# Kernel optimization log

Hardware: AMD Instinct MI355X
Metric: run time of the kernel (lower is better)

## Reference

```python
import jax, jax.numpy as jnp
import numpy as np

N_EMBD = 1024
N_HEAD = 16
HEAD_DIM = N_EMBD // N_HEAD
EPS = 1e-5


def _gelu_tanh(x):
    c = jnp.sqrt(jnp.asarray(2.0 / jnp.pi, x.dtype))
    return 0.5 * x * (1.0 + jnp.tanh(c * (x + 0.044715 * x ** 3)))


def _layernorm(x, scale, shift):
    # torch.var defaults to unbiased (ddof=1) -- replicate exactly
    mean = jnp.mean(x, axis=-1, keepdims=True)
    var = jnp.var(x, axis=-1, keepdims=True, ddof=1)
    return (x - mean) / jnp.sqrt(var + EPS) * scale + shift


def setup_inputs() -> dict:
    key = jax.random.key(0)
    ks = jax.random.split(key, 8)
    d, h = N_EMBD, 4 * N_EMBD
    s = 0.02
    return {
        "x": jax.random.normal(ks[0], (2, 2048, d), jnp.float32),
        "ln1_scale": jnp.ones((d,), jnp.float32),
        "ln1_shift": jnp.zeros((d,), jnp.float32),
        "wq": jax.random.normal(ks[1], (d, d), jnp.float32) * s,
        "wk": jax.random.normal(ks[2], (d, d), jnp.float32) * s,
        "wv": jax.random.normal(ks[3], (d, d), jnp.float32) * s,
        "w_out": jax.random.normal(ks[4], (d, d), jnp.float32) * s,
        "b_out": jnp.zeros((d,), jnp.float32),
        "ln2_scale": jnp.ones((d,), jnp.float32),
        "ln2_shift": jnp.zeros((d,), jnp.float32),
        "w1": jax.random.normal(ks[5], (d, h), jnp.float32) * s,
        "b1": jnp.zeros((h,), jnp.float32),
        "w2": jax.random.normal(ks[6], (h, d), jnp.float32) * s,
        "b2": jnp.zeros((d,), jnp.float32),
    }


def reference(x, ln1_scale, ln1_shift, wq, wk, wv, w_out, b_out,
              ln2_scale, ln2_shift, w1, b1, w2, b2):
    B, S, D = x.shape
    out = _layernorm(x, ln1_scale, ln1_shift)

    # qkv projections (no bias), split heads: [B, H, S, hd]
    q = (out @ wq).reshape(B, S, N_HEAD, HEAD_DIM).transpose(0, 2, 1, 3)
    k = (out @ wk).reshape(B, S, N_HEAD, HEAD_DIM).transpose(0, 2, 1, 3)
    v = (out @ wv).reshape(B, S, N_HEAD, HEAD_DIM).transpose(0, 2, 1, 3)

    scores = jnp.einsum("bhqd,bhkd->bhqk", q, k)
    causal = jnp.triu(jnp.ones((S, S), bool), k=1)
    # original masks BEFORE scaling; -inf / sqrt(d) is still -inf
    scores = jnp.where(causal, -jnp.inf, scores)
    weights = jax.nn.softmax(scores / jnp.sqrt(jnp.asarray(HEAD_DIM, scores.dtype)), axis=-1)
    ctx = jnp.einsum("bhqk,bhkd->bqhd", weights, v).reshape(B, S, D)
    attn_out = ctx @ w_out + b_out

    out = attn_out + x  # dropout is identity (rate 0)
    shortcut = out
    out = _layernorm(out, ln2_scale, ln2_shift)
    out = _gelu_tanh(out @ w1 + b1) @ w2 + b2
    return out + shortcut
```

## Files before the change

### kernel.cpp

```cpp
#include <hip/hip_runtime.h>
#include <stdint.h>
#include <math.h>

using bf16x8 = __attribute__((ext_vector_type(8))) short;
using f32x4  = __attribute__((ext_vector_type(4))) float;

#define MFMA16 __builtin_amdgcn_mfma_f32_16x16x32_bf16

__device__ __forceinline__ uint16_t f2b(float f) {
    union { float f; uint32_t i; } v; v.f = f;
    uint32_t r = v.i + 0x7fffu + ((v.i >> 16) & 1u);
    return (uint16_t)(r >> 16);
}
__device__ __forceinline__ float b2f(uint16_t u) {
    union { uint32_t i; float f; } v; v.i = ((uint32_t)u) << 16; return v.f;
}

typedef const __attribute__((address_space(1))) void gvoid;
typedef __attribute__((address_space(3))) void svoid;

__global__ __launch_bounds__(256) void fill_zero(float* __restrict__ o, int n) {
    int i = (blockIdx.x * 256 + threadIdx.x) * 4;
    if (i < n) *(float4*)(o + i) = make_float4(0.f, 0.f, 0.f, 0.f);
}

__global__ __launch_bounds__(256) void transpose_qkvo(
    const float* __restrict__ wq, const float* __restrict__ wk,
    const float* __restrict__ wv, const float* __restrict__ wo,
    uint16_t* __restrict__ wqkvT, uint16_t* __restrict__ woT)
{
    const int D = 1024;
    int z = blockIdx.z;
    const float* W = (z == 0) ? wq : (z == 1) ? wk : (z == 2) ? wv : wo;
    uint16_t* Wt = (z < 3) ? (wqkvT + (size_t)z * D * D) : woT;
    __shared__ uint16_t t[32][33];
    int n0 = blockIdx.x * 32, k0 = blockIdx.y * 32;
    int tx = threadIdx.x, ty = threadIdx.y;
    #pragma unroll
    for (int i = ty; i < 32; i += 8)
        t[i][tx] = f2b(W[(size_t)(k0 + i) * D + (n0 + tx)]);
    __syncthreads();
    #pragma unroll
    for (int i = ty; i < 32; i += 8)
        Wt[(size_t)(n0 + i) * D + (k0 + tx)] = t[tx][i];
}

__global__ __launch_bounds__(256) void transpose_f2b(
    const float* __restrict__ W, uint16_t* __restrict__ Wt, int K, int N)
{
    __shared__ uint16_t t[32][33];
    int n0 = blockIdx.x * 32, k0 = blockIdx.y * 32;
    int tx = threadIdx.x, ty = threadIdx.y;
    #pragma unroll
    for (int i = ty; i < 32; i += 8)
        t[i][tx] = f2b(W[(size_t)(k0 + i) * N + (n0 + tx)]);
    __syncthreads();
    #pragma unroll
    for (int i = ty; i < 32; i += 8)
        Wt[(size_t)(n0 + i) * K + (k0 + tx)] = t[tx][i];
}

__global__ __launch_bounds__(256) void ln_kernel(
    const float* __restrict__ src, const float* __restrict__ scale,
    const float* __restrict__ shift, uint16_t* __restrict__ out)
{
    const int D = 1024;
    int row = blockIdx.x, t = threadIdx.x;
    float4 f = *((const float4*)(src + (size_t)row * D) + t);
    float v[4] = {f.x, f.y, f.z, f.w};
    float s1 = v[0] + v[1] + v[2] + v[3];
    float s2 = v[0]*v[0] + v[1]*v[1] + v[2]*v[2] + v[3]*v[3];
    #pragma unroll
    for (int off = 32; off; off >>= 1) {
        s1 += __shfl_xor(s1, off);
        s2 += __shfl_xor(s2, off);
    }
    __shared__ float red[2][4];
    __shared__ float stat[2];
    int wid = t >> 6, lane = t & 63;
    if (lane == 0) { red[0][wid] = s1; red[1][wid] = s2; }
    __syncthreads();
    if (t == 0) {
        float S1 = red[0][0] + red[0][1] + red[0][2] + red[0][3];
        float S2 = red[1][0] + red[1][1] + red[1][2] + red[1][3];
        float mean = S1 / (float)D;
        float var  = fmaxf((S2 - mean * S1) / (float)(D - 1), 0.f);
        stat[0] = mean; stat[1] = rsqrtf(var + 1e-5f);
    }
    __syncthreads();
    float mean = stat[0], rstd = stat[1];
    float4 sc = *((const float4*)scale + t);
    float4 sh = *((const float4*)shift + t);
    uint16_t o[4];
    o[0] = f2b((v[0] - mean) * rstd * sc.x + sh.x);
    o[1] = f2b((v[1] - mean) * rstd * sc.y + sh.y);
    o[2] = f2b((v[2] - mean) * rstd * sc.z + sh.z);
    o[3] = f2b((v[3] - mean) * rstd * sc.w + sh.w);
    uint2 st;
    st.x = (uint32_t)o[0] | ((uint32_t)o[1] << 16);
    st.y = (uint32_t)o[2] | ((uint32_t)o[3] << 16);
    *(uint2*)(out + (size_t)row * D + t * 4) = st;
}

__global__ __launch_bounds__(256) void combine2(
    float* __restrict__ dst, const float* __restrict__ part0,
    const float* __restrict__ resid, const float* __restrict__ bias)
{
    const int D = 1024;
    size_t o = (size_t)blockIdx.x * D + threadIdx.x * 4;
    float4 a = *(float4*)(dst + o);
    float4 b = *(const float4*)(part0 + o);
    float4 c = *(const float4*)(resid + o);
    float4 bv = *((const float4*)bias + threadIdx.x);
    a.x += b.x + c.x + bv.x;
    a.y += b.y + c.y + bv.y;
    a.z += b.z + c.z + bv.z;
    a.w += b.w + c.w + bv.w;
    *(float4*)(dst + o) = a;
}

__global__ __launch_bounds__(256) void combine2ln(
    float* __restrict__ res1, const float* __restrict__ part0,
    const float* __restrict__ x, const float* __restrict__ bo,
    const float* __restrict__ scale, const float* __restrict__ shift,
    uint16_t* __restrict__ out)
{
    const int D = 1024;
    int row = blockIdx.x, t = threadIdx.x;
    size_t o = (size_t)row * D + t * 4;
    float4 a = *(float4*)(res1 + o);
    float4 b = *(const float4*)(part0 + o);
    float4 c = *(const float4*)(x + o);
    float4 bv = *((const float4*)bo + t);
    float v[4] = {a.x + b.x + c.x + bv.x, a.y + b.y + c.y + bv.y,
                  a.z + b.z + c.z + bv.z, a.w + b.w + c.w + bv.w};
    *(float4*)(res1 + o) = make_float4(v[0], v[1], v[2], v[3]);

    float s1 = v[0] + v[1] + v[2] + v[3];
    float s2 = v[0]*v[0] + v[1]*v[1] + v[2]*v[2] + v[3]*v[3];
    #pragma unroll
    for (int off = 32; off; off >>= 1) {
        s1 += __shfl_xor(s1, off);
        s2 += __shfl_xor(s2, off);
    }
    __shared__ float red[2][4];
    __shared__ float stat[2];
    int wid = t >> 6, lane = t & 63;
    if (lane == 0) { red[0][wid] = s1; red[1][wid] = s2; }
    __syncthreads();
    if (t == 0) {
        float S1 = red[0][0] + red[0][1] + red[0][2] + red[0][3];
        float S2 = red[1][0] + red[1][1] + red[1][2] + red[1][3];
        float mean = S1 / (float)D;
        float var  = fmaxf((S2 - mean * S1) / (float)(D - 1), 0.f);
        stat[0] = mean; stat[1] = rsqrtf(var + 1e-5f);
    }
    __syncthreads();
    float mean = stat[0], rstd = stat[1];
    float4 sc = *((const float4*)scale + t);
    float4 sh = *((const float4*)shift + t);
    uint16_t ob[4];
    ob[0] = f2b((v[0] - mean) * rstd * sc.x + sh.x);
    ob[1] = f2b((v[1] - mean) * rstd * sc.y + sh.y);
    ob[2] = f2b((v[2] - mean) * rstd * sc.z + sh.z);
    ob[3] = f2b((v[3] - mean) * rstd * sc.w + sh.w);
    uint2 st;
    st.x = (uint32_t)ob[0] | ((uint32_t)ob[1] << 16);
    st.y = (uint32_t)ob[2] | ((uint32_t)ob[3] << 16);
    *(uint2*)(out + (size_t)row * D + t * 4) = st;
}

__device__ __forceinline__ void stage128(
    const uint16_t* __restrict__ A, const uint16_t* __restrict__ Bt,
    uint16_t* As, uint16_t* Bs,
    int m0, int n0, int lda, int kk, int w, int l)
{
    int srow = l >> 3;
    int sc = ((l & 7) ^ srow) << 3;
    #pragma unroll
    for (int p = 0; p < 4; ++p) {
        int rbase = w * 32 + p * 8;
        const uint16_t* ga = A  + (size_t)(m0 + rbase + srow) * lda + kk + sc;
        const uint16_t* gb = Bt + (size_t)(n0 + rbase + srow) * lda + kk + sc;
        __builtin_amdgcn_global_load_lds((gvoid*)ga, (svoid*)(As + rbase * 64), 16, 0, 0);
        __builtin_amdgcn_global_load_lds((gvoid*)gb, (svoid*)(Bs + rbase * 64), 16, 0, 0);
    }
}

__device__ __forceinline__ void comp128(
    const uint16_t* As, const uint16_t* Bs, f32x4 (&acc)[4][4],
    int mo, int no, int quad, int ln, int sw)
{
    #pragma unroll
    for (int s = 0; s < 2; ++s) {
        int cc = ((s * 64 + quad * 16) ^ sw) >> 1;
        bf16x8 af[4], bf[4];
        #pragma unroll
        for (int i = 0; i < 4; ++i)
            af[i] = *(const bf16x8*)(As + (mo + i * 16 + ln) * 64 + cc);
        #pragma unroll
        for (int i = 0; i < 4; ++i)
            bf[i] = *(const bf16x8*)(Bs + (no + i * 16 + ln) * 64 + cc);
        #pragma unroll
        for (int mi = 0; mi < 4; ++mi)
            #pragma unroll
            for (int ni = 0; ni < 4; ++ni)
                acc[mi][ni] = MFMA16(af[mi], bf[ni], acc[mi][ni], 0, 0, 0);
    }
}

template <int EPI>
__global__ __launch_bounds__(256) void gemm128(
    const uint16_t* __restrict__ A, const uint16_t* __restrict__ Bt,
    const float* __restrict__ bias, const float* __restrict__ resid,
    void* __restrict__ outp, void* __restrict__ out2,
    int M, int N, int K, int lda)
{
    __shared__ __align__(16) uint16_t As0[128 * 64];
    __shared__ __align__(16) uint16_t As1[128 * 64];
    __shared__ __align__(16) uint16_t Bs0[128 * 64];
    __shared__ __align__(16) uint16_t Bs1[128 * 64];
    int tid = threadIdx.x;
    int w = tid >> 6, l = tid & 63;
    int quad = l >> 4, ln = l & 15;
    int sw = (ln & 7) << 4;

    int Nt = gridDim.x, Mt = gridDim.y;
    int L0 = blockIdx.y * Nt + blockIdx.x;
    int nb = Nt * Mt;
    int L = (L0 & 7) * (nb >> 3) + (L0 >> 3);
    const int GROUP = 8;
    int nig = GROUP * Nt;
    int gid = L / nig;
    int fm = gid * GROUP;
    int gsz = min(Mt - fm, GROUP);
    int rem = L - gid * nig;
    int pid_m = fm + rem % gsz;
    int pid_n = rem / gsz;
    int n0 = pid_n * 128, m0 = pid_m * 128;
    int kofs = (EPI == 5) ? blockIdx.z * K : 0;

    int mo = (w & 1) * 64, no = (w >> 1) * 64;

    f32x4 acc[4][4];
    #pragma unroll
    for (int mi = 0; mi < 4; ++mi)
        #pragma unroll
        for (int ni = 0; ni < 4; ++ni) acc[mi][ni] = (f32x4){0.f, 0.f, 0.f, 0.f};

    int nk = K >> 6;
    stage128(A, Bt, As0, Bs0, m0, n0, lda, kofs, w, l);
    __syncthreads();

    for (int t = 0; t + 2 <= nk; t += 2) {
        stage128(A, Bt, As1, Bs1, m0, n0, lda, kofs + (t + 1) * 64, w, l);
        comp128(As0, Bs0, acc, mo, no, quad, ln, sw);
        __syncthreads();
        if (t + 2 < nk)
            stage128(A, Bt, As0, Bs0, m0, n0, lda, kofs + (t + 2) * 64, w, l);
        comp128(As1, Bs1, acc, mo, no, quad, ln, sw);
        if (t + 2 < nk) __syncthreads();
    }

    float* pout = (EPI == 5) ? (blockIdx.z ? (float*)out2 : (float*)outp) : (float*)outp;

    #pragma unroll
    for (int ni = 0; ni < 4; ++ni) {
        int col = n0 + no + ni * 16 + ln;
        if (EPI == 4 && col >= 2048) {
            int hh = (col - 2048) >> 6, d = (col - 2048) & 63;
            #pragma unroll
            for (int mi = 0; mi < 4; ++mi) {
                int tok = m0 + mo + mi * 16 + quad * 4;
                int bat = tok >> 11, s = tok & 2047;
                uint16_t pk[4];
                #pragma unroll
                for (int r = 0; r < 4; ++r) pk[r] = f2b(acc[mi][ni][r]);
                uint2 st;
                st.x = (uint32_t)pk[0] | ((uint32_t)pk[1] << 16);
                st.y = (uint32_t)pk[2] | ((uint32_t)pk[3] << 16);
                *(uint2*)((uint16_t*)out2 +
                          ((size_t)(bat * 16 + hh) * 64 + d) * 2048 + s) = st;
            }
            continue;
        }
        float bv = (EPI == 1 || EPI == 2) ? bias[col] : 0.f;
        #pragma unroll
        for (int mi = 0; mi < 4; ++mi) {
            #pragma unroll
            for (int r = 0; r < 4; ++r) {
                int row = m0 + mo + mi * 16 + quad * 4 + r;
                float vacc = acc[mi][ni][r] + bv;
                if (EPI == 1) {
                    size_t idx = (size_t)row * N + col;
                    ((float*)outp)[idx] = vacc + resid[idx];
                } else if (EPI == 5) {
                    pout[(size_t)row * N + col] = vacc;
                } else if (EPI == 2) {
                    float x = vacc;
                    float u = 0.7978845608028654f * (x + 0.044715f * x * x * x);
                    float g = x / (1.f + __expf(-2.f * u));
                    ((uint16_t*)outp)[(size_t)row * N + col] = f2b(g);
                } else {
                    float vs = (col < 1024) ? vacc * 0.125f : vacc;
                    ((uint16_t*)outp)[(size_t)(col >> 10) * M * 1024 +
                                      (size_t)row * 1024 + (col & 1023)] = f2b(vs);
                }
            }
        }
    }
}

__device__ __forceinline__ void stage_half(
    const uint16_t* __restrict__ Mat, uint16_t* lds,
    int panel0, int lda, int kk, int w, int l)
{
    #pragma unroll
    for (int i = 0; i < 2; ++i) {
        int idx = i * 512 + w * 64 + l;
        int row = idx >> 3;
        int sc = ((idx & 7) ^ (row & 7)) << 3;
        const uint16_t* g = Mat + (size_t)(panel0 + row) * lda + kk + sc;
        __builtin_amdgcn_global_load_lds(
            (gvoid*)g, (svoid*)(lds + (i * 512 + w * 64) * 8), 16, 0, 0);
    }
}

template <int EPI>
__global__ __launch_bounds__(512, 2) void gemm256(
    const uint16_t* __restrict__ A, const uint16_t* __restrict__ Bt,
    const float* __restrict__ bias, const float* __restrict__ resid,
    void* __restrict__ outp, void* __restrict__ out2,
    int M, int N, int K, int lda)
{
    __shared__ __align__(16) uint16_t AsL[32768];
    __shared__ __align__(16) uint16_t BsL[32768];
    int tid = threadIdx.x;
    int w = tid >> 6, l = tid & 63;
    int quad = l >> 4, ln = l & 15;
    int wr = w >> 2, wc = w & 3;
    int sw = (ln & 7) << 4;
    int cc0 = ((quad * 16) ^ sw) >> 1;
    int cc1 = ((64 + quad * 16) ^ sw) >> 1;

    int Nt = gridDim.x, Mt = gridDim.y;
    int L0 = blockIdx.y * Nt + blockIdx.x;
    int nb = Nt * Mt;
    int L = (L0 & 7) * (nb >> 3) + (L0 >> 3);
    const int GROUP = 8;
    int nig = GROUP * Nt;
    int gid = L / nig;
    int fm = gid * GROUP;
    int gsz = min(Mt - fm, GROUP);
    int rem = L - gid * nig;
    int pid_m = fm + rem % gsz;
    int pid_n = rem / gsz;
    int n0 = pid_n * 256, m0 = pid_m * 256;
    int kofs = (EPI == 5) ? blockIdx.z * K : 0;

    f32x4 acc[8][4];
    #pragma unroll
    for (int mi = 0; mi < 8; ++mi)
        #pragma unroll
        for (int ni = 0; ni < 4; ++ni) acc[mi][ni] = (f32x4){0.f, 0.f, 0.f, 0.f};

    int nk = K >> 6;

    stage_half(Bt, BsL,         n0,       lda, kofs,      w, l);
    stage_half(A,  AsL,         m0,       lda, kofs,      w, l);
    stage_half(A,  AsL + 8192,  m0 + 128, lda, kofs,      w, l);
    stage_half(Bt, BsL + 8192,  n0 + 128, lda, kofs,      w, l);
    stage_half(Bt, BsL + 16384, n0,       lda, kofs + 64, w, l);
    stage_half(A,  AsL + 16384, m0,       lda, kofs + 64, w, l);
    asm volatile("s_waitcnt vmcnt(4)" ::: "memory");
    __builtin_amdgcn_s_barrier();
    __builtin_amdgcn_sched_barrier(0);

    for (int t = 0; t < nk; ++t) {
        int b = t & 1;
        const uint16_t* Ar = AsL + b * 16384 + wr * 8192;
        const uint16_t* Br = BsL + b * 16384 + (wc >> 1) * 8192 + (wc & 1) * 4096;
        uint16_t* stA1 = AsL + (b ^ 1) * 16384 + 8192;
        uint16_t* stB1 = BsL + (b ^ 1) * 16384 + 8192;
        uint16_t* stA0 = AsL + b * 16384;
        uint16_t* stB0 = BsL + b * 16384;
        int kk1 = kofs + (t + 1) * 64;
        int kk2 = kofs + (t + 2) * 64;
        bool g1 = (t + 1) < nk, g2 = (t + 2) < nk;

        bf16x8 af[4][2], bL[2][2], bH[2][2];

        #pragma unroll
        for (int mi = 0; mi < 4; ++mi) {
            af[mi][0] = *(const bf16x8*)(Ar + (mi * 16 + ln) * 64 + cc0);
            af[mi][1] = *(const bf16x8*)(Ar + (mi * 16 + ln) * 64 + cc1);
        }
        #pragma unroll
        for (int ni = 0; ni < 2; ++ni) {
            bL[ni][0] = *(const bf16x8*)(Br + (ni * 16 + ln) * 64 + cc0);
            bL[ni][1] = *(const bf16x8*)(Br + (ni * 16 + ln) * 64 + cc1);
        }
        if (g1) stage_half(A, stA1, m0 + 128, lda, kk1, w, l);
        __builtin_amdgcn_s_barrier();
        __builtin_amdgcn_sched_barrier(0);
        __builtin_amdgcn_s_setprio(1);
        #pragma unroll
        for (int mi = 0; mi < 4; ++mi)
            #pragma unroll
            for (int ni = 0; ni < 2; ++ni) {
                acc[mi][ni] = MFMA16(af[mi][0], bL[ni][0], acc[mi][ni], 0, 0, 0);
                acc[mi][ni] = MFMA16(af[mi][1], bL[ni][1], acc[mi][ni], 0, 0, 0);
            }
        __builtin_amdgcn_s_setprio(0);
        __builtin_amdgcn_s_barrier();
        __builtin_amdgcn_sched_barrier(0);

        #pragma unroll
        for (int ni = 0; ni < 2; ++ni) {
            bH[ni][0] = *(const bf16x8*)(Br + ((ni + 2) * 16 + ln) * 64 + cc0);
            bH[ni][1] = *(const bf16x8*)(Br + ((ni + 2) * 16 + ln) * 64 + cc1);
        }
        if (g1) stage_half(Bt, stB1, n0 + 128, lda, kk1, w, l);
        __builtin_amdgcn_s_barrier();
        __builtin_amdgcn_sched_barrier(0);
        __builtin_amdgcn_s_setprio(1);
        #pragma unroll
        for (int mi = 0; mi < 4; ++mi)
            #pragma unroll
            for (int ni = 0; ni < 2; ++ni) {
                acc[mi][ni + 2] = MFMA16(af[mi][0], bH[ni][0], acc[mi][ni + 2], 0, 0, 0);
                acc[mi][ni + 2] = MFMA16(af[mi][1], bH[ni][1], acc[mi][ni + 2], 0, 0, 0);
            }
        __builtin_amdgcn_s_setprio(0);
        __builtin_amdgcn_s_barrier();
        __builtin_amdgcn_sched_barrier(0);

        #pragma unroll
        for (int mi = 0; mi < 4; ++mi) {
            af[mi][0] = *(const bf16x8*)(Ar + ((mi + 4) * 16 + ln) * 64 + cc0);
            af[mi][1] = *(const bf16x8*)(Ar + ((mi + 4) * 16 + ln) * 64 + cc1);
        }
        if (g2) stage_half(Bt, stB0, n0, lda, kk2, w, l);
        __builtin_amdgcn_s_barrier();
        __builtin_amdgcn_sched_barrier(0);
        __builtin_amdgcn_s_setprio(1);
        #pragma unroll
        for (int mi = 0; mi < 4; ++mi)
            #pragma unroll
            for (int ni = 0; ni < 2; ++ni) {
                acc[mi + 4][ni] = MFMA16(af[mi][0], bL[ni][0], acc[mi + 4][ni], 0, 0, 0);
                acc[mi + 4][ni] = MFMA16(af[mi][1], bL[ni][1], acc[mi + 4][ni], 0, 0, 0);
            }
        __builtin_amdgcn_s_setprio(0);
        __builtin_amdgcn_s_barrier();
        __builtin_amdgcn_sched_barrier(0);

        if (g2) {
            stage_half(A, stA0, m0, lda, kk2, w, l);
            asm volatile("s_waitcnt vmcnt(4)" ::: "memory");
        } else if (g1) {
            asm volatile("s_waitcnt vmcnt(0)" ::: "memory");
        }
        __builtin_amdgcn_s_barrier();
        __builtin_amdgcn_sched_barrier(0);
        __builtin_amdgcn_s_setprio(1);
        #pragma unroll
        for (int mi = 0; mi < 4; ++mi)
            #pragma unroll
            for (int ni = 0; ni < 2; ++ni) {
                acc[mi + 4][ni + 2] = MFMA16(af[mi][0], bH[ni][0], acc[mi + 4][ni + 2], 0, 0, 0);
                acc[mi + 4][ni + 2] = MFMA16(af[mi][1], bH[ni][1], acc[mi + 4][ni + 2], 0, 0, 0);
            }
        __builtin_amdgcn_s_setprio(0);
        __builtin_amdgcn_s_barrier();
        __builtin_amdgcn_sched_barrier(0);
    }

    float* pout = (EPI == 5) ? (blockIdx.z ? (float*)out2 : (float*)outp) : (float*)outp;

    #pragma unroll
    for (int ni = 0; ni < 4; ++ni) {
        int col = n0 + wc * 64 + ni * 16 + ln;
        if (EPI == 4 && col >= 2048) {
            int hh = (col - 2048) >> 6, d = (col - 2048) & 63;
            #pragma unroll
            for (int mi = 0; mi < 8; ++mi) {
                int tok = m0 + wr * 128 + mi * 16 + quad * 4;
                int bat = tok >> 11, s = tok & 2047;
                uint16_t pk[4];
                #pragma unroll
                for (int r = 0; r < 4; ++r) pk[r] = f2b(acc[mi][ni][r]);
                uint2 st;
                st.x = (uint32_t)pk[0] | ((uint32_t)pk[1] << 16);
                st.y = (uint32_t)pk[2] | ((uint32_t)pk[3] << 16);
                *(uint2*)((uint16_t*)out2 +
                          ((size_t)(bat * 16 + hh) * 64 + d) * 2048 + s) = st;
            }
            continue;
        }
        float bv = (EPI == 2) ? bias[col] : 0.f;
        #pragma unroll
        for (int mi = 0; mi < 8; ++mi) {
            #pragma unroll
            for (int r = 0; r < 4; ++r) {
                int row = m0 + wr * 128 + mi * 16 + quad * 4 + r;
                float vacc = acc[mi][ni][r] + bv;
                if (EPI == 5) {
                    pout[(size_t)row * N + col] = vacc;
                } else if (EPI == 2) {
                    float x = vacc;
                    float u = 0.7978845608028654f * (x + 0.044715f * x * x * x);
                    float g = x / (1.f + __expf(-2.f * u));
                    ((uint16_t*)outp)[(size_t)row * N + col] = f2b(g);
                } else {
                    float vs = (col < 1024) ? vacc * 0.125f : vacc;
                    ((uint16_t*)outp)[(size_t)(col >> 10) * M * 1024 +
                                      (size_t)row * 1024 + (col & 1023)] = f2b(vs);
                }
            }
        }
    }
}

__device__ __forceinline__ void attn_tile(
    const uint16_t* __restrict__ Kl, const uint16_t* __restrict__ Vl,
    uint16_t* __restrict__ Pw,
    bf16x8 qf0, bf16x8 qf1,
    float* l_r, f32x4* o_acc,
    int qw, int kv0, bool diag, int quad, int ln)
{
    const int LW = 72;
    f32x4 sf[4];
    #pragma unroll
    for (int nt2 = 0; nt2 < 4; ++nt2) {
        const uint16_t* kp = Kl + (nt2 * 16 + ln) * LW + quad * 8;
        bf16x8 k0 = *(const bf16x8*)(kp);
        bf16x8 k1 = *(const bf16x8*)(kp + 32);
        f32x4 z = {0.f, 0.f, 0.f, 0.f};
        z = MFMA16(qf0, k0, z, 0, 0, 0);
        z = MFMA16(qf1, k1, z, 0, 0, 0);
        sf[nt2] = z;
    }
    #pragma unroll
    for (int r = 0; r < 4; ++r) {
        float ps = 0.f;
        if (diag) {
            int qrow = qw + quad * 4 + r;
            #pragma unroll
            for (int nt2 = 0; nt2 < 4; ++nt2) {
                int kv = kv0 + nt2 * 16 + ln;
                float pv = (kv <= qrow) ? __expf(sf[nt2][r]) : 0.f;
                sf[nt2][r] = pv;
                ps += pv;
            }
        } else {
            #pragma unroll
            for (int nt2 = 0; nt2 < 4; ++nt2) {
                float pv = __expf(sf[nt2][r]);
                sf[nt2][r] = pv;
                ps += pv;
            }
        }
        ps += __shfl_xor(ps, 1);
        ps += __shfl_xor(ps, 2);
        ps += __shfl_xor(ps, 4);
        ps += __shfl_xor(ps, 8);
        l_r[r] += ps;
    }
    #pragma unroll
    for (int nt2 = 0; nt2 < 4; ++nt2) {
        int gl = nt2 * 2 + (ln >> 3);
        int off = ln & 7;
        #pragma unroll
        for (int r = 0; r < 4; ++r) {
            int row = quad * 4 + r;
            int p = gl ^ ((quad << 1) ^ r);
            Pw[row * 64 + p * 8 + off] = f2b(sf[nt2][r]);
        }
    }
    int swl = ((ln >> 2) << 1) ^ (ln & 3);
    int g0 = quad ^ swl;
    int g1 = (quad + 4) ^ swl;
    bf16x8 p0 = *(const bf16x8*)(Pw + ln * 64 + g0 * 8);
    bf16x8 p1 = *(const bf16x8*)(Pw + ln * 64 + g1 * 8);
    #pragma unroll
    for (int dt = 0; dt < 4; ++dt) {
        const uint16_t* vp = Vl + (dt * 16 + ln) * LW + quad * 8;
        bf16x8 v0 = *(const bf16x8*)(vp);
        bf16x8 v1 = *(const bf16x8*)(vp + 32);
        o_acc[dt] = MFMA16(p0, v0, o_acc[dt], 0, 0, 0);
        o_acc[dt] = MFMA16(p1, v1, o_acc[dt], 0, 0, 0);
    }
}

__global__ __launch_bounds__(256) void attn_flash(
    const uint16_t* __restrict__ Q,
    const uint16_t* __restrict__ K,
    const uint16_t* __restrict__ Vt,
    uint16_t* __restrict__ O,
    int B, int S, int H)
{
    const int D = 1024;
    const int LW = 72;
    __shared__ uint16_t Kl[64 * 72];
    __shared__ uint16_t Vl[64 * 72];
    __shared__ uint16_t Pl[64 * 64];

    int tid = threadIdx.x;
    int w = tid >> 6, l = tid & 63;
    int quad = l >> 4, ln = l & 15;

    int NT = S / 64;
    int h = blockIdx.y, b = blockIdx.z;
    int qt = ((h >> 3) & 1) ? blockIdx.x : (NT - 1 - blockIdx.x);
    size_t rb = (size_t)b * S;

    int qw = qt * 64 + w * 16;

    const uint16_t* qp = Q + (rb + qw + ln) * D + h * 64 + quad * 8;
    bf16x8 q0 = *(const bf16x8*)(qp);
    bf16x8 q1 = *(const bf16x8*)(qp + 32);

    const uint16_t* Kbase = K + rb * D + h * 64;
    const uint16_t* Vbase = Vt + (size_t)(b * H + h) * 64 * S;
    uint16_t* Pw = Pl + w * 16 * 64;

    int sr0 = tid >> 3,         sc0 = (tid & 7) * 8;
    int sr1 = (256 + tid) >> 3, sc1 = ((256 + tid) & 7) * 8;

    float lr[4] = {0.f, 0.f, 0.f, 0.f};
    f32x4 oa[4];
    #pragma unroll
    for (int dt = 0; dt < 4; ++dt)
        oa[dt] = (f32x4){0.f, 0.f, 0.f, 0.f};

    uint4 kr0 = *(const uint4*)(Kbase + (size_t)sr0 * D + sc0);
    uint4 kr1 = *(const uint4*)(Kbase + (size_t)sr1 * D + sc1);
    uint4 vr0 = *(const uint4*)(Vbase + (size_t)sr0 * S + sc0);
    uint4 vr1 = *(const uint4*)(Vbase + (size_t)sr1 * S + sc1);

    for (int t = 0; t <= qt; ++t) {
        __syncthreads();
        *(uint4*)(Kl + sr0 * LW + sc0) = kr0;
        *(uint4*)(Kl + sr1 * LW + sc1) = kr1;
        *(uint4*)(Vl + sr0 * LW + sc0) = vr0;
        *(uint4*)(Vl + sr1 * LW + sc1) = vr1;
        __syncthreads();
        if (t < qt) {
            int kv1 = (t + 1) * 64;
            kr0 = *(const uint4*)(Kbase + (size_t)(kv1 + sr0) * D + sc0);
            kr1 = *(const uint4*)(Kbase + (size_t)(kv1 + sr1) * D + sc1);
            vr0 = *(const uint4*)(Vbase + (size_t)sr0 * S + kv1 + sc0);
            vr1 = *(const uint4*)(Vbase + (size_t)sr1 * S + kv1 + sc1);
        }
        attn_tile(Kl, Vl, Pw, q0, q1, lr, oa, qw, t * 64, t == qt, quad, ln);
    }

    #pragma unroll
    for (int r = 0; r < 4; ++r) {
        float inv = 1.f / lr[r];
        uint16_t* op = O + (rb + qw + quad * 4 + r) * D + h * 64 + ln;
        #pragma unroll
        for (int dt = 0; dt < 4; ++dt)
            op[dt * 16] = f2b(oa[dt][r] * inv);
    }
}

extern "C" void kernel_launch(void* const* d_in, const int* in_sizes, int n_in,
                              void* d_out, int out_size, void* d_ws, size_t ws_size,
                              hipStream_t stream)
{
    (void)in_sizes; (void)n_in;
    const int B = 2, S = 2048, D = 1024, H = 16, F = 4096;
    const int M = B * S;
    const size_t MB = 1u << 20;

    const float* x    = (const float*)d_in[0];
    const float* ln1s = (const float*)d_in[1];
    const float* ln1b = (const float*)d_in[2];
    const float* wq   = (const float*)d_in[3];
    const float* wk   = (const float*)d_in[4];
    const float* wv   = (const float*)d_in[5];
    const float* wo   = (const float*)d_in[6];
    const float* bo   = (const float*)d_in[7];
    const float* ln2s = (const float*)d_in[8];
    const float* ln2b = (const float*)d_in[9];
    const float* w1   = (const float*)d_in[10];
    const float* b1   = (const float*)d_in[11];
    const float* w2   = (const float*)d_in[12];
    const float* b2   = (const float*)d_in[13];

    if (ws_size < 56 * MB) {
        fill_zero<<<(out_size + 1023) / 1024, 256, 0, stream>>>((float*)d_out, out_size);
        return;
    }
    bool full = ws_size >= 72 * MB;

    char* base = (char*)d_ws;
    uint16_t* woT    = (uint16_t*)(base + 0 * MB);
    uint16_t* wqkvT  = (uint16_t*)(base + 2 * MB);
    uint16_t* ln1o   = (uint16_t*)(base + 8 * MB);
    uint16_t* qb     = (uint16_t*)(base + 16 * MB);
    uint16_t* vbT    = (uint16_t*)(base + 32 * MB);
    uint16_t* ctx    = (uint16_t*)(base + 40 * MB);
    uint16_t* kb     = (uint16_t*)(base + 24 * MB);
    uint16_t* w1T    = (uint16_t*)(base + 0 * MB);
    float*    res1   = (float*)   (base + (full ? 56 : 16) * MB);
    uint16_t* ln2o   = (uint16_t*)(base + (full ? 8 : 32) * MB);
    uint16_t* w2T    = (uint16_t*)(base + (full ? 16 : 40) * MB);
    uint16_t* h1     = (uint16_t*)(base + (full ? 24 : 48) * MB);
    float*    part0  = (float*)   (base + 0 * MB);
    float*    partP  = (float*)   (base + 8 * MB);

    dim3 tb(32, 8);
    transpose_qkvo<<<dim3(D / 32, D / 32, 4), tb, 0, stream>>>(
        wq, wk, wv, wo, wqkvT, woT);

    ln_kernel<<<M, 256, 0, stream>>>(x, ln1s, ln1b, ln1o);

    if (full) {
        gemm256<4><<<dim3(3072 / 256, M / 256), 512, 0, stream>>>(
            ln1o, wqkvT, nullptr, nullptr, qb, vbT, M, 3072, D, D);
    } else {
        gemm128<4><<<dim3(3072 / 128, M / 128), 256, 0, stream>>>(
            ln1o, wqkvT, nullptr, nullptr, qb, vbT, M, 3072, D, D);
    }

    attn_flash<<<dim3(S / 64, H, B), 256, 0, stream>>>(qb, kb, vbT, ctx, B, S, H);

    if (full) {
        gemm256<5><<<dim3(D / 256, M / 256, 2), 512, 0, stream>>>(
            ctx, woT, nullptr, nullptr, partP, res1, M, D, D / 2, D);
        combine2ln<<<M, 256, 0, stream>>>(res1, partP, x, bo, ln2s, ln2b, ln2o);
    } else {
        gemm128<1><<<dim3(D / 128, M / 128), 256, 0, stream>>>(
            ctx, woT, bo, x, res1, nullptr, M, D, D, D);
        ln_kernel<<<M, 256, 0, stream>>>(res1, ln2s, ln2b, ln2o);
    }

    transpose_f2b<<<dim3(F / 32, D / 32), tb, 0, stream>>>(w1, w1T, D, F);
    transpose_f2b<<<dim3(D / 32, F / 32), tb, 0, stream>>>(w2, w2T, F, D);

    if (full) {
        gemm256<2><<<dim3(F / 256, M / 256), 512, 0, stream>>>(
            ln2o, w1T, b1, nullptr, h1, nullptr, M, F, D, D);
        gemm256<5><<<dim3(D / 256, M / 256, 2), 512, 0, stream>>>(
            h1, w2T, nullptr, nullptr, part0, d_out, M, D, F / 2, F);
        combine2<<<M, 256, 0, stream>>>((float*)d_out, part0, res1, b2);
    } else {
        const int MH = M / 2;
        for (int half = 0; half < 2; ++half) {
            size_t ro = (size_t)half * MH;
            gemm128<2><<<dim3(F / 128, MH / 128), 256, 0, stream>>>(
                ln2o + ro * D, w1T, b1, nullptr, h1, nullptr, MH, F, D, D);
            gemm128<1><<<dim3(D / 128, MH / 128), 256, 0, stream>>>(
                h1, w2T, b2, res1 + ro * D, (float*)d_out + ro * D, nullptr, MH, D, F, F);
        }
    }
}
```

Measured before the change: 392.1 us.

## Pair causal query tiles per block and split KV tiles across two wave groups

Each attention block now handles one low and one high query tile together, so the total causal work per block is the same everywhere. The block grows to 512 threads, split into two 4-wave groups that take alternating KV tiles from separate shared-memory buffers. At the end the two groups merge their partial output accumulators and row sums through shared memory. The aim is to remove causal load imbalance and the tail effect, at the cost of extra syncs, a merge step and more shared memory and registers per block.

```diff
diff --git a/kernel.cpp b/kernel.cpp
--- a/kernel.cpp
+++ b/kernel.cpp
@@ -593,7 +593,7 @@
     }
 }
 
-__global__ __launch_bounds__(256) void attn_flash(
+__global__ __launch_bounds__(512, 4) void attn_flash(
     const uint16_t* __restrict__ Q,
     const uint16_t* __restrict__ K,
     const uint16_t* __restrict__ Vt,
@@ -602,67 +602,142 @@
 {
     const int D = 1024;
     const int LW = 72;
-    __shared__ uint16_t Kl[64 * 72];
-    __shared__ uint16_t Vl[64 * 72];
-    __shared__ uint16_t Pl[64 * 64];
+    __shared__ __align__(16) uint16_t smem[26624];
 
     int tid = threadIdx.x;
     int w = tid >> 6, l = tid & 63;
+    int g = w >> 2, wq = w & 3;
     int quad = l >> 4, ln = l & 15;
 
     int NT = S / 64;
     int h = blockIdx.y, b = blockIdx.z;
-    int qt = ((h >> 3) & 1) ? blockIdx.x : (NT - 1 - blockIdx.x);
+    int qlo = blockIdx.x, qhi = NT - 1 - qlo;
     size_t rb = (size_t)b * S;
 
-    int qw = qt * 64 + w * 16;
-
-    const uint16_t* qp = Q + (rb + qw + ln) * D + h * 64 + quad * 8;
-    bf16x8 q0 = *(const bf16x8*)(qp);
-    bf16x8 q1 = *(const bf16x8*)(qp + 32);
-
-    const uint16_t* Kbase = K + rb * D + h * 64;
-    const uint16_t* Vbase = Vt + (size_t)(b * H + h) * 64 * S;
-    uint16_t* Pw = Pl + w * 16 * 64;
-
-    int sr0 = tid >> 3,         sc0 = (tid & 7) * 8;
-    int sr1 = (256 + tid) >> 3, sc1 = ((256 + tid) & 7) * 8;
-
-    float lr[4] = {0.f, 0.f, 0.f, 0.f};
-    f32x4 oa[4];
-    #pragma unroll
-    for (int dt = 0; dt < 4; ++dt)
-        oa[dt] = (f32x4){0.f, 0.f, 0.f, 0.f};
-
-    uint4 kr0 = *(const uint4*)(Kbase + (size_t)sr0 * D + sc0);
-    uint4 kr1 = *(const uint4*)(Kbase + (size_t)sr1 * D + sc1);
-    uint4 vr0 = *(const uint4*)(Vbase + (size_t)sr0 * S + sc0);
-    uint4 vr1 = *(const uint4*)(Vbase + (size_t)sr1 * S + sc1);
-
-    for (int t = 0; t <= qt; ++t) {
-        __syncthreads();
-        *(uint4*)(Kl + sr0 * LW + sc0) = kr0;
-        *(uint4*)(Kl + sr1 * LW + sc1) = kr1;
-        *(uint4*)(Vl + sr0 * LW + sc0) = vr0;
-        *(uint4*)(Vl + sr1 * LW + sc1) = vr1;
-        __syncthreads();
-        if (t < qt) {
-            int kv1 = (t + 1) * 64;
-            kr0 = *(const uint4*)(Kbase + (size_t)(kv1 + sr0) * D + sc0);
-            kr1 = *(const uint4*)(Kbase + (size_t)(kv1 + sr1) * D + sc1);
-            vr0 = *(const uint4*)(Vbase + (size_t)sr0 * S + kv1 + sc0);
-            vr1 = *(const uint4*)(Vbase + (size_t)sr1 * S + kv1 + sc1);
-        }
-        attn_tile(Kl, Vl, Pw, q0, q1, lr, oa, qw, t * 64, t == qt, quad, ln);
-    }
-
-    #pragma unroll
-    for (int r = 0; r < 4; ++r) {
-        float inv = 1.f / lr[r];
-        uint16_t* op = O + (rb + qw + quad * 4 + r) * D + h * 64 + ln;
+    int qwh = qhi * 64 + wq * 16;
+    int qwl = qlo * 64 + wq * 16;
+
+    uint16_t* Kg = smem + g * 4608;
+    uint16_t* Vg = smem + 9216 + g * 4608;
+    uint16_t* Pw = smem + 18432 + w * 1024;
+
+    const uint16_t* qph = Q + (rb + qwh + ln) * D + h * 64 + quad * 8;
+    bf16x8 qh0 = *(const bf16x8*)(qph);
+    bf16x8 qh1 = *(const bf16x8*)(qph + 32);
+    const uint16_t* qpl = Q + (rb + qwl + ln) * D + h * 64 + quad * 8;
+    bf16x8 ql0 = *(const bf16x8*)(qpl);
+    bf16x8 ql1 = *(const bf16x8*)(qpl + 32);
+
+    const uint16_t* Kb = K + rb * D + h * 64;
+    const uint16_t* Vb = Vt + (size_t)(b * H + h) * 64 * S;
+
+    int t256 = tid & 255;
+    int sr0 = t256 >> 3, sc0 = (t256 & 7) * 8;
+    int sr1 = sr0 + 32;
+
+    int nH = (qhi + 2 - g) >> 1;
+    int nL = (qlo + 2 - g) >> 1;
+    int my_ns = nH + nL;
+
+    float lH[4] = {0.f, 0.f, 0.f, 0.f};
+    float lL[4] = {0.f, 0.f, 0.f, 0.f};
+    f32x4 oH[4], oL[4];
+    #pragma unroll
+    for (int dt = 0; dt < 4; ++dt) {
+        oH[dt] = (f32x4){0.f, 0.f, 0.f, 0.f};
+        oL[dt] = (f32x4){0.f, 0.f, 0.f, 0.f};
+    }
+
+    {
+        int kv1 = g * 64;
+        uint4 kr0 = *(const uint4*)(Kb + (size_t)(kv1 + sr0) * D + sc0);
+        uint4 kr1 = *(const uint4*)(Kb + (size_t)(kv1 + sr1) * D + sc0);
+        uint4 vr0 = *(const uint4*)(Vb + (size_t)sr0 * S + kv1 + sc0);
+        uint4 vr1 = *(const uint4*)(Vb + (size_t)sr1 * S + kv1 + sc0);
+
+        for (int s = 0; s < 17; ++s) {
+            bool act = s < my_ns;
+            int t = 0;
+            if (act) t = (s < nH) ? (2 * s + g) : (2 * (s - nH) + g);
+            __syncthreads();
+            if (act) {
+                *(uint4*)(Kg + sr0 * LW + sc0) = kr0;
+                *(uint4*)(Kg + sr1 * LW + sc0) = kr1;
+                *(uint4*)(Vg + sr0 * LW + sc0) = vr0;
+                *(uint4*)(Vg + sr1 * LW + sc0) = vr1;
+            }
+            __syncthreads();
+            if (s + 1 < my_ns) {
+                int sn = s + 1;
+                int tn = (sn < nH) ? (2 * sn + g) : (2 * (sn - nH) + g);
+                int kv1n = tn * 64;
+                kr0 = *(const uint4*)(Kb + (size_t)(kv1n + sr0) * D + sc0);
+                kr1 = *(const uint4*)(Kb + (size_t)(kv1n + sr1) * D + sc0);
+                vr0 = *(const uint4*)(Vb + (size_t)sr0 * S + kv1n + sc0);
+                vr1 = *(const uint4*)(Vb + (size_t)sr1 * S + kv1n + sc0);
+            }
+            if (act) {
+                if (s < nH)
+                    attn_tile(Kg, Vg, Pw, qh0, qh1, lH, oH, qwh, t * 64,
+                              t == qhi, quad, ln);
+                else
+                    attn_tile(Kg, Vg, Pw, ql0, ql1, lL, oL, qwl, t * 64,
+                              t == qlo, quad, ln);
+            }
+        }
+    }
+
+    float* scO = (float*)smem;
+    float* scL = (float*)smem + 4096;
+    int mi = wq * 64 + l;
+
+    __syncthreads();
+    if (g == 1) {
         #pragma unroll
         for (int dt = 0; dt < 4; ++dt)
-            op[dt * 16] = f2b(oa[dt][r] * inv);
+            *(f32x4*)(scO + (mi * 4 + dt) * 4) = oH[dt];
+        #pragma unroll
+        for (int r = 0; r < 4; ++r) scL[mi * 4 + r] = lH[r];
+    }
+    __syncthreads();
+    if (g == 0) {
+        #pragma unroll
+        for (int dt = 0; dt < 4; ++dt)
+            oH[dt] += *(const f32x4*)(scO + (mi * 4 + dt) * 4);
+        #pragma unroll
+        for (int r = 0; r < 4; ++r) lH[r] += scL[mi * 4 + r];
+        #pragma unroll
+        for (int r = 0; r < 4; ++r) {
+            float inv = 1.f / lH[r];
+            uint16_t* op = O + (rb + qwh + quad * 4 + r) * D + h * 64 + ln;
+            #pragma unroll
+            for (int dt = 0; dt < 4; ++dt)
+                op[dt * 16] = f2b(oH[dt][r] * inv);
+        }
+    }
+    __syncthreads();
+    if (g == 0) {
+        #pragma unroll
+        for (int dt = 0; dt < 4; ++dt)
+            *(f32x4*)(scO + (mi * 4 + dt) * 4) = oL[dt];
+        #pragma unroll
+        for (int r = 0; r < 4; ++r) scL[mi * 4 + r] = lL[r];
+    }
+    __syncthreads();
+    if (g == 1) {
+        #pragma unroll
+        for (int dt = 0; dt < 4; ++dt)
+            oL[dt] += *(const f32x4*)(scO + (mi * 4 + dt) * 4);
+        #pragma unroll
+        for (int r = 0; r < 4; ++r) lL[r] += scL[mi * 4 + r];
+        #pragma unroll
+        for (int r = 0; r < 4; ++r) {
+            float inv = 1.f / lL[r];
+            uint16_t* op = O + (rb + qwl + quad * 4 + r) * D + h * 64 + ln;
+            #pragma unroll
+            for (int dt = 0; dt < 4; ++dt)
+                op[dt * 16] = f2b(oL[dt][r] * inv);
+        }
     }
 }
 
@@ -726,7 +801,7 @@
             ln1o, wqkvT, nullptr, nullptr, qb, vbT, M, 3072, D, D);
     }
 
-    attn_flash<<<dim3(S / 64, H, B), 256, 0, stream>>>(qb, kb, vbT, ctx, B, S, H);
+    attn_flash<<<dim3(S / 128, H, B), 512, 0, stream>>>(qb, kb, vbT, ctx, B, S, H);
 
     if (full) {
         gemm256<5><<<dim3(D / 256, M / 256, 2), 512, 0, stream>>>(
```

Result: slower. 422.4 us (+7.7%).
